# Performance work log

Measured on AMD Instinct MI355X. Metric: run time of the kernel, lower is better.

The kernel has to match this reference:

```python
import jax, jax.numpy as jnp
import numpy as np

_DIMS = [15, 30, 60, 90, 120, 90, 60, 30, 15, 10, 5, 1]


def setup_inputs() -> dict:
    key = jax.random.key(0)
    keys = jax.random.split(key, 1 + 2 * 11)
    inp = {"x": jax.random.normal(keys[0], (524288, 15), dtype=jnp.float32)}
    for i in range(11):
        fan_in, fan_out = _DIMS[i], _DIMS[i + 1]
        bound = 1.0 / np.sqrt(fan_in)
        inp[f"W{i+1}"] = jax.random.uniform(keys[1 + 2 * i], (fan_out, fan_in), minval=-bound, maxval=bound, dtype=jnp.float32)
        inp[f"b{i+1}"] = jax.random.uniform(keys[2 + 2 * i], (fan_out,), minval=-bound, maxval=bound, dtype=jnp.float32)
    return inp


def reference(x, W1, b1, W2, b2, W3, b3, W4, b4, W5, b5, W6, b6, W7, b7, W8, b8, W9, b9, W10, b10, W11, b11):
    Ws = [W1, W2, W3, W4, W5, W6, W7, W8, W9, W10, W11]
    bs = [b1, b2, b3, b4, b5, b6, b7, b8, b9, b10, b11]
    h = x
    # 10 Linear+ReLU layers, funnel 15->30->60->90->120->90->60->30->15->10->5
    for W, b in zip(Ws[:-1], bs[:-1]):
        h = jax.nn.relu(h @ W.T + b)
    # final Linear 5->1 + sigmoid
    return jax.nn.sigmoid(h @ Ws[-1].T + bs[-1])
```

## Files before the change

### kernel.cpp

```cpp
#include <hip/hip_runtime.h>
#include <math.h>


using bf16x8 = __attribute__((ext_vector_type(8))) short;
using f32x4  = __attribute__((ext_vector_type(4))) float;
using u16x4  = __attribute__((ext_vector_type(4))) unsigned short;
using u16x8  = __attribute__((ext_vector_type(8))) unsigned short;

namespace {
constexpr int NL = 11;
constexpr int IN_[NL]   = {15, 30, 60, 90, 120, 90, 60, 30, 15, 10, 5};
constexpr int OUT_[NL]  = {30, 60, 90, 120, 90, 60, 30, 15, 10, 5, 1};
constexpr int KP_[NL]   = {32, 32, 64, 96, 128, 96, 64, 32, 32, 32, 32};
constexpr int NP_[NL]   = {32, 64, 96, 128, 96, 64, 32, 16, 16, 16, 16};
constexpr int WOFF_[NL] = {0, 1024, 3072, 9216, 21504, 33792, 39936, 41984, 42496, 43008, 43520};
constexpr int WTOT      = 44032;
constexpr int BOFF_[NL] = {0, 32, 96, 192, 320, 416, 480, 512, 528, 544, 560};
constexpr int BTOT      = 576;
constexpr int ACT_OFF   = (WTOT * 2 + BTOT * 4) / 2;
constexpr int WAVES     = 8;
constexpr int ROWS_PER_WAVE  = 32;
constexpr int ROWS_PER_BLOCK = WAVES * ROWS_PER_WAVE;
constexpr int ARENA     = 4096;
constexpr int LDS_BYTES = WTOT * 2 + BTOT * 4 + WAVES * ARENA * 2;
}

__device__ __forceinline__ unsigned short f2bf(float f) {
    unsigned u = __float_as_uint(f);
    u += 0x7fffu + ((u >> 16) & 1u);
    return (unsigned short)(u >> 16);
}

template <int L>
__device__ __forceinline__ void stage_w(const float* __restrict__ W,
                                        const float* __restrict__ B,
                                        short* wlds, float* blds, int tid) {
    constexpr int KP = KP_[L], NP = NP_[L], INl = IN_[L], OUTl = OUT_[L];
    constexpr int NKT = KP / 32;
    for (int idx = tid; idx < NP * KP; idx += 512) {
        const int f    = idx >> 9;
        const int t    = idx & 511;
        const int quad = t >> 7;
        const int col  = (t >> 3) & 15;
        const int j    = t & 7;
        const int mt   = f / NKT;
        const int kt   = f - mt * NKT;
        const int m    = mt * 16 + col;
        const int k    = kt * 32 + quad * 8 + j;
        float v = (m < OUTl && k < INl) ? W[m * INl + k] : 0.f;
        wlds[WOFF_[L] + idx] = (short)f2bf(v);
    }
    for (int idx = tid; idx < NP; idx += 512)
        blds[BOFF_[L] + idx] = (idx < OUTl) ? B[idx] : 0.f;
}

template <int L>
__device__ __forceinline__ void layer_fwd(const short* __restrict__ wlds,
                                          const float* __restrict__ blds,
                                          short* buf, int col, int quad) {
    constexpr int KP   = KP_[L];
    constexpr int NP   = NP_[L];
    constexpr int NKT  = KP / 32;
    constexpr int NMT  = NP / 16;
    constexpr int KPN  = KP_[L + 1];
    constexpr int NKTN = KPN / 32;

    bf16x8 bfr[2][NKT];
#pragma unroll
    for (int b = 0; b < 2; ++b)
#pragma unroll
        for (int kt = 0; kt < NKT; ++kt)
            bfr[b][kt] = *(const bf16x8*)(buf + (b * NKT + kt) * 512 + quad * 128 + col * 8);

#pragma unroll
    for (int mt = 0; mt < NMT; ++mt) {
        f32x4 acc0 = {0.f, 0.f, 0.f, 0.f};
        f32x4 acc1 = {0.f, 0.f, 0.f, 0.f};
#pragma unroll
        for (int kt = 0; kt < NKT; ++kt) {
            bf16x8 af = *(const bf16x8*)(wlds + WOFF_[L] + (mt * NKT + kt) * 512 + quad * 128 + col * 8);
            acc0 = __builtin_amdgcn_mfma_f32_16x16x32_bf16(af, bfr[0][kt], acc0, 0, 0, 0);
            acc1 = __builtin_amdgcn_mfma_f32_16x16x32_bf16(af, bfr[1][kt], acc1, 0, 0, 0);
        }
        f32x4 bias = *(const f32x4*)(blds + BOFF_[L] + mt * 16 + quad * 4);
        const int wbase = (mt >> 1) * 512 + ((mt & 1) * 2 + (quad >> 1)) * 128 + col * 8 + (quad & 1) * 4;
#pragma unroll
        for (int b = 0; b < 2; ++b) {
            u16x4 o;
#pragma unroll
            for (int r = 0; r < 4; ++r) {
                float v = (b ? acc1[r] : acc0[r]) + bias[r];
                v = fmaxf(v, 0.f);
                o[r] = f2bf(v);
            }
            *(u16x4*)(buf + b * NKTN * 512 + wbase) = o;
        }
    }
    if constexpr (NP < KPN) {
        u16x8 z = {0, 0, 0, 0, 0, 0, 0, 0};
        *(u16x8*)(buf + (quad >> 1) * NKTN * 512 + (2 + (quad & 1)) * 128 + col * 8) = z;
    }
}

extern "C" __global__ void __launch_bounds__(512, 1)
mlp_fused(const float* __restrict__ x,
          const float* __restrict__ W0,  const float* __restrict__ B0,
          const float* __restrict__ W1,  const float* __restrict__ B1,
          const float* __restrict__ W2,  const float* __restrict__ B2,
          const float* __restrict__ W3,  const float* __restrict__ B3,
          const float* __restrict__ W4,  const float* __restrict__ B4,
          const float* __restrict__ W5,  const float* __restrict__ B5,
          const float* __restrict__ W6,  const float* __restrict__ B6,
          const float* __restrict__ W7,  const float* __restrict__ B7,
          const float* __restrict__ W8,  const float* __restrict__ B8,
          const float* __restrict__ W9,  const float* __restrict__ B9,
          const float* __restrict__ W10, const float* __restrict__ B10,
          float* __restrict__ out, int nchunks) {
    extern __shared__ short smem[];
    short* wlds = smem;
    float* blds = (float*)(smem + WTOT);
    short* act  = smem + ACT_OFF;

    const int tid = threadIdx.x;

    stage_w<0>(W0, B0, wlds, blds, tid);
    stage_w<1>(W1, B1, wlds, blds, tid);
    stage_w<2>(W2, B2, wlds, blds, tid);
    stage_w<3>(W3, B3, wlds, blds, tid);
    stage_w<4>(W4, B4, wlds, blds, tid);
    stage_w<5>(W5, B5, wlds, blds, tid);
    stage_w<6>(W6, B6, wlds, blds, tid);
    stage_w<7>(W7, B7, wlds, blds, tid);
    stage_w<8>(W8, B8, wlds, blds, tid);
    stage_w<9>(W9, B9, wlds, blds, tid);
    stage_w<10>(W10, B10, wlds, blds, tid);
    __syncthreads();

    const int wave = tid >> 6;
    const int lane = tid & 63;
    const int col  = lane & 15;
    const int quad = lane >> 4;
    short* buf = act + wave * ARENA;

    for (int chunk = blockIdx.x; chunk < nchunks; chunk += gridDim.x) {
        const int row0 = chunk * ROWS_PER_BLOCK + wave * ROWS_PER_WAVE;

#pragma unroll
        for (int b = 0; b < 2; ++b) {
            const int row = row0 + b * 16 + col;
            const float* xr = x + (long)row * 15;
            float v[4];
            if (quad < 3) {
                float4 t;
                __builtin_memcpy(&t, xr + quad * 4, 16);
                v[0] = t.x; v[1] = t.y; v[2] = t.z; v[3] = t.w;
            } else {
                v[0] = xr[12]; v[1] = xr[13]; v[2] = xr[14]; v[3] = 0.f;
            }
            u16x4 o;
#pragma unroll
            for (int r = 0; r < 4; ++r) o[r] = f2bf(v[r]);
            *(u16x4*)(buf + b * 512 + (quad >> 1) * 128 + col * 8 + (quad & 1) * 4) = o;
        }
        {
            u16x8 z = {0, 0, 0, 0, 0, 0, 0, 0};
            *(u16x8*)(buf + (quad >> 1) * 512 + (2 + (quad & 1)) * 128 + col * 8) = z;
        }

        layer_fwd<0>(wlds, blds, buf, col, quad);
        layer_fwd<1>(wlds, blds, buf, col, quad);
        layer_fwd<2>(wlds, blds, buf, col, quad);
        layer_fwd<3>(wlds, blds, buf, col, quad);
        layer_fwd<4>(wlds, blds, buf, col, quad);
        layer_fwd<5>(wlds, blds, buf, col, quad);
        layer_fwd<6>(wlds, blds, buf, col, quad);
        layer_fwd<7>(wlds, blds, buf, col, quad);
        layer_fwd<8>(wlds, blds, buf, col, quad);
        layer_fwd<9>(wlds, blds, buf, col, quad);

        {
            bf16x8 af = *(const bf16x8*)(wlds + WOFF_[10] + quad * 128 + col * 8);
            bf16x8 b0 = *(const bf16x8*)(buf + quad * 128 + col * 8);
            bf16x8 b1 = *(const bf16x8*)(buf + 512 + quad * 128 + col * 8);
            f32x4 acc0 = {0.f, 0.f, 0.f, 0.f};
            f32x4 acc1 = {0.f, 0.f, 0.f, 0.f};
            acc0 = __builtin_amdgcn_mfma_f32_16x16x32_bf16(af, b0, acc0, 0, 0, 0);
            acc1 = __builtin_amdgcn_mfma_f32_16x16x32_bf16(af, b1, acc1, 0, 0, 0);
            if (quad == 0) {
                const float bias0 = blds[BOFF_[10]];
                const float z0 = acc0[0] + bias0;
                const float z1 = acc1[0] + bias0;
                out[row0 + col]      = 1.f / (1.f + __expf(-z0));
                out[row0 + 16 + col] = 1.f / (1.f + __expf(-z1));
            }
        }
    }
}

extern "C" void kernel_launch(void* const* d_in, const int* in_sizes, int n_in,
                              void* d_out, int out_size, void* d_ws, size_t ws_size,
                              hipStream_t stream) {
    (void)n_in; (void)d_ws; (void)ws_size; (void)out_size;
    const float* x = (const float*)d_in[0];
    const float* W[11];
    const float* B[11];
    for (int i = 0; i < 11; ++i) {
        W[i] = (const float*)d_in[1 + 2 * i];
        B[i] = (const float*)d_in[2 + 2 * i];
    }
    const int nrows   = in_sizes[0] / 15;
    const int nchunks = nrows / ROWS_PER_BLOCK;

    hipFuncSetAttribute((const void*)mlp_fused,
                        hipFuncAttributeMaxDynamicSharedMemorySize, LDS_BYTES);

    mlp_fused<<<dim3(256), dim3(512), LDS_BYTES, stream>>>(
        x,
        W[0], B[0], W[1], B[1], W[2], B[2], W[3], B[3], W[4], B[4],
        W[5], B[5], W[6], B[6], W[7], B[7], W[8], B[8], W[9], B[9],
        W[10], B[10],
        (float*)d_out, nchunks);
}
```

Baseline: 198.4 us.

## Fold biases into augmented weights, prefetch inputs, keep small-layer weights in registers

Each layer's bias moves into an extra input column of the padded weight tile. The bias is stored as a bf16 hi/lo pair against a constant-one activation lane, which removes the separate bias load and add in every layer epilogue. The layer loop is reordered to iterate k outermost with all accumulators live. Packed bf16 conversion replaces manual rounding, the next chunk's x rows are prefetched during compute, and the four tiny tail layers' weights are held in registers. Occupancy hint rises to two blocks per CU, but LDS use (~150KB per block) and the larger register footprint may prevent that.

```diff
diff --git a/kernel.cpp b/kernel.cpp
--- a/kernel.cpp
+++ b/kernel.cpp
@@ -4,8 +4,9 @@
 
 using bf16x8 = __attribute__((ext_vector_type(8))) short;
 using f32x4  = __attribute__((ext_vector_type(4))) float;
-using u16x4  = __attribute__((ext_vector_type(4))) unsigned short;
 using u16x8  = __attribute__((ext_vector_type(8))) unsigned short;
+using u32x2  = __attribute__((ext_vector_type(2))) unsigned;
+typedef __bf16 bf16x2_t __attribute__((ext_vector_type(2)));
 
 namespace {
 constexpr int NL = 11;
@@ -15,14 +16,11 @@
 constexpr int NP_[NL]   = {32, 64, 96, 128, 96, 64, 32, 16, 16, 16, 16};
 constexpr int WOFF_[NL] = {0, 1024, 3072, 9216, 21504, 33792, 39936, 41984, 42496, 43008, 43520};
 constexpr int WTOT      = 44032;
-constexpr int BOFF_[NL] = {0, 32, 96, 192, 320, 416, 480, 512, 528, 544, 560};
-constexpr int BTOT      = 576;
-constexpr int ACT_OFF   = (WTOT * 2 + BTOT * 4) / 2;
+constexpr int ACT_OFF   = WTOT;
 constexpr int WAVES     = 8;
-constexpr int ROWS_PER_WAVE  = 32;
-constexpr int ROWS_PER_BLOCK = WAVES * ROWS_PER_WAVE;
+constexpr int ROWS_PER_BLOCK = WAVES * 32;
 constexpr int ARENA     = 4096;
-constexpr int LDS_BYTES = WTOT * 2 + BTOT * 4 + WAVES * ARENA * 2;
+constexpr int LDS_BYTES = (WTOT + WAVES * ARENA) * 2;
 }
 
 __device__ __forceinline__ unsigned short f2bf(float f) {
@@ -31,32 +29,50 @@
     return (unsigned short)(u >> 16);
 }
 
+__device__ __forceinline__ unsigned pk2(float a, float b) {
+#if __has_builtin(__builtin_amdgcn_cvt_pk_bf16_f32)
+    return __builtin_bit_cast(unsigned, __builtin_amdgcn_cvt_pk_bf16_f32(a, b));
+#else
+    bf16x2_t c;
+    c[0] = (__bf16)a;
+    c[1] = (__bf16)b;
+    return __builtin_bit_cast(unsigned, c);
+#endif
+}
+
 template <int L>
 __device__ __forceinline__ void stage_w(const float* __restrict__ W,
                                         const float* __restrict__ B,
-                                        short* wlds, float* blds, int tid) {
+                                        short* wlds, int tid) {
     constexpr int KP = KP_[L], NP = NP_[L], INl = IN_[L], OUTl = OUT_[L];
     constexpr int NKT = KP / 32;
     for (int idx = tid; idx < NP * KP; idx += 512) {
         const int f    = idx >> 9;
         const int t    = idx & 511;
         const int quad = t >> 7;
-        const int col  = (t >> 3) & 15;
+        const int colc = (t >> 3) & 15;
         const int j    = t & 7;
         const int mt   = f / NKT;
         const int kt   = f - mt * NKT;
-        const int m    = mt * 16 + col;
+        const int m    = mt * 16 + colc;
         const int k    = kt * 32 + quad * 8 + j;
-        float v = (m < OUTl && k < INl) ? W[m * INl + k] : 0.f;
+        float v = 0.f;
+        if (m < OUTl) {
+            if (k < INl) v = W[m * INl + k];
+            else if (k == INl) v = B[m];
+            else if (k == INl + 1) {
+                float hf = __builtin_bit_cast(float, (unsigned)f2bf(B[m]) << 16);
+                v = B[m] - hf;
+            }
+        } else if (m == OUTl || m == OUTl + 1) {
+            if (k == INl) v = 1.f;
+        }
         wlds[WOFF_[L] + idx] = (short)f2bf(v);
     }
-    for (int idx = tid; idx < NP; idx += 512)
-        blds[BOFF_[L] + idx] = (idx < OUTl) ? B[idx] : 0.f;
 }
 
 template <int L>
 __device__ __forceinline__ void layer_fwd(const short* __restrict__ wlds,
-                                          const float* __restrict__ blds,
                                           short* buf, int col, int quad) {
     constexpr int KP   = KP_[L];
     constexpr int NP   = NP_[L];
@@ -64,45 +80,100 @@
     constexpr int NMT  = NP / 16;
     constexpr int KPN  = KP_[L + 1];
     constexpr int NKTN = KPN / 32;
-
-    bf16x8 bfr[2][NKT];
-#pragma unroll
-    for (int b = 0; b < 2; ++b)
-#pragma unroll
-        for (int kt = 0; kt < NKT; ++kt)
-            bfr[b][kt] = *(const bf16x8*)(buf + (b * NKT + kt) * 512 + quad * 128 + col * 8);
-
+    const short* wl = wlds + WOFF_[L];
+    const int fo = quad * 128 + col * 8;
+
+    f32x4 acc[NMT][2];
+#pragma unroll
+    for (int mt = 0; mt < NMT; ++mt)
+#pragma unroll
+        for (int b = 0; b < 2; ++b)
+            acc[mt][b] = f32x4{0.f, 0.f, 0.f, 0.f};
+
+#pragma unroll
+    for (int kt = 0; kt < NKT; ++kt) {
+        bf16x8 b0 = *(const bf16x8*)(buf + kt * 512 + fo);
+        bf16x8 b1 = *(const bf16x8*)(buf + (NKT + kt) * 512 + fo);
+#pragma unroll
+        for (int mt = 0; mt < NMT; ++mt) {
+            bf16x8 af = *(const bf16x8*)(wl + (mt * NKT + kt) * 512 + fo);
+            acc[mt][0] = __builtin_amdgcn_mfma_f32_16x16x32_bf16(af, b0, acc[mt][0], 0, 0, 0);
+            acc[mt][1] = __builtin_amdgcn_mfma_f32_16x16x32_bf16(af, b1, acc[mt][1], 0, 0, 0);
+        }
+    }
 #pragma unroll
     for (int mt = 0; mt < NMT; ++mt) {
-        f32x4 acc0 = {0.f, 0.f, 0.f, 0.f};
-        f32x4 acc1 = {0.f, 0.f, 0.f, 0.f};
-#pragma unroll
-        for (int kt = 0; kt < NKT; ++kt) {
-            bf16x8 af = *(const bf16x8*)(wlds + WOFF_[L] + (mt * NKT + kt) * 512 + quad * 128 + col * 8);
-            acc0 = __builtin_amdgcn_mfma_f32_16x16x32_bf16(af, bfr[0][kt], acc0, 0, 0, 0);
-            acc1 = __builtin_amdgcn_mfma_f32_16x16x32_bf16(af, bfr[1][kt], acc1, 0, 0, 0);
-        }
-        f32x4 bias = *(const f32x4*)(blds + BOFF_[L] + mt * 16 + quad * 4);
         const int wbase = (mt >> 1) * 512 + ((mt & 1) * 2 + (quad >> 1)) * 128 + col * 8 + (quad & 1) * 4;
 #pragma unroll
         for (int b = 0; b < 2; ++b) {
-            u16x4 o;
-#pragma unroll
-            for (int r = 0; r < 4; ++r) {
-                float v = (b ? acc1[r] : acc0[r]) + bias[r];
-                v = fmaxf(v, 0.f);
-                o[r] = f2bf(v);
-            }
-            *(u16x4*)(buf + b * NKTN * 512 + wbase) = o;
+            u32x2 o;
+            o[0] = pk2(fmaxf(acc[mt][b][0], 0.f), fmaxf(acc[mt][b][1], 0.f));
+            o[1] = pk2(fmaxf(acc[mt][b][2], 0.f), fmaxf(acc[mt][b][3], 0.f));
+            *(u32x2*)(buf + b * NKTN * 512 + wbase) = o;
         }
     }
     if constexpr (NP < KPN) {
         u16x8 z = {0, 0, 0, 0, 0, 0, 0, 0};
+        if ((quad & 1) == 0) z[0] = (unsigned short)0x3F80;
         *(u16x8*)(buf + (quad >> 1) * NKTN * 512 + (2 + (quad & 1)) * 128 + col * 8) = z;
     }
 }
 
-extern "C" __global__ void __launch_bounds__(512, 1)
+__device__ __forceinline__ void layer_one(bf16x8 af, short* buf, int col, int quad) {
+    const int fo = quad * 128 + col * 8;
+    bf16x8 b0 = *(const bf16x8*)(buf + fo);
+    bf16x8 b1 = *(const bf16x8*)(buf + 512 + fo);
+    f32x4 a0 = f32x4{0.f, 0.f, 0.f, 0.f};
+    f32x4 a1 = f32x4{0.f, 0.f, 0.f, 0.f};
+    a0 = __builtin_amdgcn_mfma_f32_16x16x32_bf16(af, b0, a0, 0, 0, 0);
+    a1 = __builtin_amdgcn_mfma_f32_16x16x32_bf16(af, b1, a1, 0, 0, 0);
+    const int wbase = (quad >> 1) * 128 + col * 8 + (quad & 1) * 4;
+    u32x2 o0, o1;
+    o0[0] = pk2(fmaxf(a0[0], 0.f), fmaxf(a0[1], 0.f));
+    o0[1] = pk2(fmaxf(a0[2], 0.f), fmaxf(a0[3], 0.f));
+    o1[0] = pk2(fmaxf(a1[0], 0.f), fmaxf(a1[1], 0.f));
+    o1[1] = pk2(fmaxf(a1[2], 0.f), fmaxf(a1[3], 0.f));
+    *(u32x2*)(buf + wbase) = o0;
+    *(u32x2*)(buf + 512 + wbase) = o1;
+    u16x8 z = {0, 0, 0, 0, 0, 0, 0, 0};
+    if ((quad & 1) == 0) z[0] = (unsigned short)0x3F80;
+    *(u16x8*)(buf + (quad >> 1) * 512 + (2 + (quad & 1)) * 128 + col * 8) = z;
+}
+
+__device__ __forceinline__ float4 ld4(const float* p) {
+    float4 t;
+    __builtin_memcpy(&t, p, 16);
+    return t;
+}
+
+__device__ __forceinline__ void fetch_x(const float* __restrict__ x, int row0,
+                                        int col, int quad, float4& a0, float4& a1) {
+    const float* r0 = x + (long)(row0 + col) * 15;
+    const float* r1 = x + (long)(row0 + 16 + col) * 15;
+    if (quad < 3) {
+        a0 = ld4(r0 + quad * 4);
+        a1 = ld4(r1 + quad * 4);
+    } else {
+        float4 t0 = ld4(r0 + 11), t1 = ld4(r1 + 11);
+        a0 = make_float4(t0.y, t0.z, t0.w, 1.f);
+        a1 = make_float4(t1.y, t1.z, t1.w, 1.f);
+    }
+}
+
+__device__ __forceinline__ void stage_x(short* buf, float4 a0, float4 a1,
+                                        int col, int quad) {
+    const int off = (quad >> 1) * 128 + col * 8 + (quad & 1) * 4;
+    u32x2 o0, o1;
+    o0[0] = pk2(a0.x, a0.y); o0[1] = pk2(a0.z, a0.w);
+    o1[0] = pk2(a1.x, a1.y); o1[1] = pk2(a1.z, a1.w);
+    *(u32x2*)(buf + off) = o0;
+    *(u32x2*)(buf + 512 + off) = o1;
+    u16x8 z = {0, 0, 0, 0, 0, 0, 0, 0};
+    if ((quad & 1) == 0) z[0] = (unsigned short)0x3F80;
+    *(u16x8*)(buf + (quad >> 1) * 512 + (2 + (quad & 1)) * 128 + col * 8) = z;
+}
+
+extern "C" __global__ void __launch_bounds__(512, 2)
 mlp_fused(const float* __restrict__ x,
           const float* __restrict__ W0,  const float* __restrict__ B0,
           const float* __restrict__ W1,  const float* __restrict__ B1,
@@ -118,22 +189,21 @@
           float* __restrict__ out, int nchunks) {
     extern __shared__ short smem[];
     short* wlds = smem;
-    float* blds = (float*)(smem + WTOT);
     short* act  = smem + ACT_OFF;
 
     const int tid = threadIdx.x;
 
-    stage_w<0>(W0, B0, wlds, blds, tid);
-    stage_w<1>(W1, B1, wlds, blds, tid);
-    stage_w<2>(W2, B2, wlds, blds, tid);
-    stage_w<3>(W3, B3, wlds, blds, tid);
-    stage_w<4>(W4, B4, wlds, blds, tid);
-    stage_w<5>(W5, B5, wlds, blds, tid);
-    stage_w<6>(W6, B6, wlds, blds, tid);
-    stage_w<7>(W7, B7, wlds, blds, tid);
-    stage_w<8>(W8, B8, wlds, blds, tid);
-    stage_w<9>(W9, B9, wlds, blds, tid);
-    stage_w<10>(W10, B10, wlds, blds, tid);
+    stage_w<0>(W0, B0, wlds, tid);
+    stage_w<1>(W1, B1, wlds, tid);
+    stage_w<2>(W2, B2, wlds, tid);
+    stage_w<3>(W3, B3, wlds, tid);
+    stage_w<4>(W4, B4, wlds, tid);
+    stage_w<5>(W5, B5, wlds, tid);
+    stage_w<6>(W6, B6, wlds, tid);
+    stage_w<7>(W7, B7, wlds, tid);
+    stage_w<8>(W8, B8, wlds, tid);
+    stage_w<9>(W9, B9, wlds, tid);
+    stage_w<10>(W10, B10, wlds, tid);
     __syncthreads();
 
     const int wave = tid >> 6;
@@ -141,57 +211,47 @@
     const int col  = lane & 15;
     const int quad = lane >> 4;
     short* buf = act + wave * ARENA;
-
-    for (int chunk = blockIdx.x; chunk < nchunks; chunk += gridDim.x) {
-        const int row0 = chunk * ROWS_PER_BLOCK + wave * ROWS_PER_WAVE;
-
-#pragma unroll
-        for (int b = 0; b < 2; ++b) {
-            const int row = row0 + b * 16 + col;
-            const float* xr = x + (long)row * 15;
-            float v[4];
-            if (quad < 3) {
-                float4 t;
-                __builtin_memcpy(&t, xr + quad * 4, 16);
-                v[0] = t.x; v[1] = t.y; v[2] = t.z; v[3] = t.w;
-            } else {
-                v[0] = xr[12]; v[1] = xr[13]; v[2] = xr[14]; v[3] = 0.f;
-            }
-            u16x4 o;
-#pragma unroll
-            for (int r = 0; r < 4; ++r) o[r] = f2bf(v[r]);
-            *(u16x4*)(buf + b * 512 + (quad >> 1) * 128 + col * 8 + (quad & 1) * 4) = o;
-        }
+    const int fo = quad * 128 + col * 8;
+
+    const bf16x8 w7  = *(const bf16x8*)(wlds + WOFF_[7]  + fo);
+    const bf16x8 w8  = *(const bf16x8*)(wlds + WOFF_[8]  + fo);
+    const bf16x8 w9  = *(const bf16x8*)(wlds + WOFF_[9]  + fo);
+    const bf16x8 w10 = *(const bf16x8*)(wlds + WOFF_[10] + fo);
+
+    int chunk = blockIdx.x;
+    float4 xa, xb;
+    if (chunk < nchunks)
+        fetch_x(x, chunk * ROWS_PER_BLOCK + wave * 32, col, quad, xa, xb);
+
+    for (; chunk < nchunks; chunk += gridDim.x) {
+        const int row0 = chunk * ROWS_PER_BLOCK + wave * 32;
+        stage_x(buf, xa, xb, col, quad);
+
+        const int nxt = chunk + gridDim.x;
+        if (nxt < nchunks)
+            fetch_x(x, nxt * ROWS_PER_BLOCK + wave * 32, col, quad, xa, xb);
+
+        layer_fwd<0>(wlds, buf, col, quad);
+        layer_fwd<1>(wlds, buf, col, quad);
+        layer_fwd<2>(wlds, buf, col, quad);
+        layer_fwd<3>(wlds, buf, col, quad);
+        layer_fwd<4>(wlds, buf, col, quad);
+        layer_fwd<5>(wlds, buf, col, quad);
+        layer_fwd<6>(wlds, buf, col, quad);
+        layer_one(w7, buf, col, quad);
+        layer_one(w8, buf, col, quad);
+        layer_one(w9, buf, col, quad);
+
         {
-            u16x8 z = {0, 0, 0, 0, 0, 0, 0, 0};
-            *(u16x8*)(buf + (quad >> 1) * 512 + (2 + (quad & 1)) * 128 + col * 8) = z;
-        }
-
-        layer_fwd<0>(wlds, blds, buf, col, quad);
-        layer_fwd<1>(wlds, blds, buf, col, quad);
-        layer_fwd<2>(wlds, blds, buf, col, quad);
-        layer_fwd<3>(wlds, blds, buf, col, quad);
-        layer_fwd<4>(wlds, blds, buf, col, quad);
-        layer_fwd<5>(wlds, blds, buf, col, quad);
-        layer_fwd<6>(wlds, blds, buf, col, quad);
-        layer_fwd<7>(wlds, blds, buf, col, quad);
-        layer_fwd<8>(wlds, blds, buf, col, quad);
-        layer_fwd<9>(wlds, blds, buf, col, quad);
-
-        {
-            bf16x8 af = *(const bf16x8*)(wlds + WOFF_[10] + quad * 128 + col * 8);
-            bf16x8 b0 = *(const bf16x8*)(buf + quad * 128 + col * 8);
-            bf16x8 b1 = *(const bf16x8*)(buf + 512 + quad * 128 + col * 8);
-            f32x4 acc0 = {0.f, 0.f, 0.f, 0.f};
-            f32x4 acc1 = {0.f, 0.f, 0.f, 0.f};
-            acc0 = __builtin_amdgcn_mfma_f32_16x16x32_bf16(af, b0, acc0, 0, 0, 0);
-            acc1 = __builtin_amdgcn_mfma_f32_16x16x32_bf16(af, b1, acc1, 0, 0, 0);
+            bf16x8 b0 = *(const bf16x8*)(buf + fo);
+            bf16x8 b1 = *(const bf16x8*)(buf + 512 + fo);
+            f32x4 a0 = f32x4{0.f, 0.f, 0.f, 0.f};
+            f32x4 a1 = f32x4{0.f, 0.f, 0.f, 0.f};
+            a0 = __builtin_amdgcn_mfma_f32_16x16x32_bf16(w10, b0, a0, 0, 0, 0);
+            a1 = __builtin_amdgcn_mfma_f32_16x16x32_bf16(w10, b1, a1, 0, 0, 0);
             if (quad == 0) {
-                const float bias0 = blds[BOFF_[10]];
-                const float z0 = acc0[0] + bias0;
-                const float z1 = acc1[0] + bias0;
-                out[row0 + col]      = 1.f / (1.f + __expf(-z0));
-                out[row0 + 16 + col] = 1.f / (1.f + __expf(-z1));
+                out[row0 + col]      = 1.f / (1.f + __expf(-a0[0]));
+                out[row0 + 16 + col] = 1.f / (1.f + __expf(-a1[0]));
             }
         }
     }
```

New measurement: 196.8 us. Within noise of the previous version (-0.8%).
